# Optimization experiments

Hardware: AMD Instinct MI355X
Metric: run time of the kernel (lower is better)

## Reference

```python
import jax, jax.numpy as jnp
import numpy as np

N_WORDS, MAX_CHARS = 32768, 16
WORD_DIM, CHAR_DIM, HIDDEN = 256, 64, 256
VOCAB = 256


def setup_inputs() -> dict:
    key = jax.random.key(0)
    ks = jax.random.split(key, 10)
    char_indices = jax.random.randint(ks[0], (N_WORDS, MAX_CHARS), 0, VOCAB)
    char_lengths = jax.random.randint(ks[1], (N_WORDS,), 1, MAX_CHARS + 1)
    word_emb = jax.random.normal(ks[2], (N_WORDS, WORD_DIM), dtype=jnp.float32)
    s = 0.05
    E_char = jax.random.normal(ks[3], (VOCAB, CHAR_DIM), dtype=jnp.float32) * s
    W_ih = jax.random.normal(ks[4], (4 * HIDDEN, CHAR_DIM), dtype=jnp.float32) * s
    W_hh = jax.random.normal(ks[5], (4 * HIDDEN, HIDDEN), dtype=jnp.float32) * s
    b_ih = jax.random.normal(ks[6], (4 * HIDDEN,), dtype=jnp.float32) * s
    b_hh = jax.random.normal(ks[7], (4 * HIDDEN,), dtype=jnp.float32) * s
    W_lin = jax.random.normal(ks[8], (WORD_DIM, WORD_DIM + HIDDEN), dtype=jnp.float32) * s
    b_lin = jax.random.normal(ks[9], (WORD_DIM,), dtype=jnp.float32) * s
    return dict(char_indices=char_indices, char_lengths=char_lengths,
                word_emb=word_emb, E_char=E_char, W_ih=W_ih, W_hh=W_hh,
                b_ih=b_ih, b_hh=b_hh, W_lin=W_lin, b_lin=b_lin)


def _lstm_last_hidden(x, lengths, W_ih, W_hh, b_ih, b_hh):
    # x: [N, T, E]; returns final hidden h at position length-1 per row.
    N, T, _ = x.shape
    H = W_hh.shape[1]
    x_proj = jnp.einsum('nte,ge->ntg', x, W_ih) + (b_ih + b_hh)  # [N, T, 4H]
    x_proj = jnp.transpose(x_proj, (1, 0, 2))                    # time-major [T, N, 4H]

    def step(carry, inp):
        h, c = carry
        xg, t = inp
        gates = xg + h @ W_hh.T
        i, f, g, o = jnp.split(gates, 4, axis=-1)
        i, f, o = jax.nn.sigmoid(i), jax.nn.sigmoid(f), jax.nn.sigmoid(o)
        g = jnp.tanh(g)
        c_new = f * c + i * g
        h_new = o * jnp.tanh(c_new)
        mask = (t < lengths)[:, None]  # freeze state past each word's length
        h = jnp.where(mask, h_new, h)
        c = jnp.where(mask, c_new, c)
        return (h, c), None

    h0 = jnp.zeros((N, H), dtype=x.dtype)
    c0 = jnp.zeros((N, H), dtype=x.dtype)
    (h, _), _ = jax.lax.scan(step, (h0, c0), (x_proj, jnp.arange(T)))
    return h


def reference(char_indices, char_lengths, word_emb, E_char, W_ih, W_hh,
              b_ih, b_hh, W_lin, b_lin):
    char_embedded = E_char[char_indices]                        # [N, T, E]
    h = _lstm_last_hidden(char_embedded, char_lengths, W_ih, W_hh, b_ih, b_hh)
    combined = jnp.concatenate([word_emb, h], axis=-1)          # [N, WORD+H]
    return jax.nn.relu(combined @ W_lin.T + b_lin)              # [N, WORD]
```

## Files before the change

kernel.cpp:

```cpp
#include <hip/hip_runtime.h>


#define NW 32768

typedef __attribute__((ext_vector_type(8))) short short8;
typedef __attribute__((ext_vector_type(4))) float f32x4;
typedef __attribute__((ext_vector_type(4))) int i32x4;
typedef __attribute__((ext_vector_type(4))) unsigned short u16x4;

#define MFMA16(a,b,c) __builtin_amdgcn_mfma_f32_16x16x32_bf16(a,b,c,0,0,0)
#define MFMAI8(a,b,c) __builtin_amdgcn_mfma_i32_16x16x32_i8(a,b,c,0,0,0)

#define O_ORDER 0
#define O_SLEN  131072
#define O_WPK   262144
#define O_USTP  524288
#define O_WLIN  528384
#define O_PX    790528
#define O_BH    1314816
#define O_BASE  1323008

__device__ inline unsigned short f2b(float f) {
  unsigned u = __builtin_bit_cast(unsigned, f);
  u = u + 0x7fffu + ((u >> 16) & 1u);
  return (unsigned short)(u >> 16);
}
__device__ inline float b2f(unsigned short u) {
  return __builtin_bit_cast(float, ((unsigned)u) << 16);
}
__device__ inline float fsigm(float x) {
  float e = __builtin_amdgcn_exp2f(-1.44269504f * x);
  return __builtin_amdgcn_rcpf(1.0f + e);
}
__device__ inline float ftanh(float x) {
  float e = __builtin_amdgcn_exp2f(2.88539008f * x);
  return 1.0f - 2.0f * __builtin_amdgcn_rcpf(e + 1.0f);
}

__global__ void k_prep0(const float* __restrict__ whh, unsigned char* __restrict__ ws) {
  int i = blockIdx.x * 256 + threadIdx.x;
  const f32x4* r4 = (const f32x4*)(whh + i * 256);
  float mx = 0.f;
  #pragma unroll 8
  for (int k4 = 0; k4 < 64; ++k4) {
    f32x4 v = r4[k4];
    mx = fmaxf(mx, fmaxf(fmaxf(fabsf(v[0]), fabsf(v[1])),
                         fmaxf(fabsf(v[2]), fabsf(v[3]))));
  }
  ((float*)(ws + O_USTP))[i] = mx / (127.f * 127.f);
}

__global__ void k_prep1(const float* __restrict__ whh, const float* __restrict__ wlin,
                        unsigned char* __restrict__ ws) {
  int i = blockIdx.x * 256 + threadIdx.x;
  if (i < 262144) {
    int j = i & 7, lane = (i >> 3) & 63, t2 = i >> 9;
    int nt = t2 & 7, u2 = t2 >> 3;
    int kb = u2 & 7, w = u2 >> 3;
    int n = (nt >> 1) * 256 + w * 32 + (nt & 1) * 16 + (lane & 15);
    int k = kb * 32 + (lane >> 4) * 8 + j;
    float v = whh[n * 256 + k];
    float ustep = ((const float*)(ws + O_USTP))[n] * 127.f;
    float qf = (ustep > 0.f) ? v / ustep : 0.f;
    int q = (int)__builtin_rintf(qf);
    q = q < -127 ? -127 : (q > 127 ? 127 : q);
    ((signed char*)(ws + O_WPK))[i] = (signed char)q;
    return;
  }
  int i2 = i - 262144;
  {
    int j = i2 & 7, lane = (i2 >> 3) & 63, t3 = i2 >> 9;
    int kf = t3 & 15, nn = t3 >> 4;
    int n = (nn >> 2) * 64 + (nn & 3) * 16 + (lane & 15);
    int k = kf * 32 + (lane >> 4) * 8 + j;
    ((unsigned short*)(ws + O_WLIN))[i2] = f2b(wlin[n * 512 + k]);
  }
}

__global__ void k_prep2(const float* __restrict__ wih, const float* __restrict__ ech,
                        const float* __restrict__ bih, const float* __restrict__ bhh,
                        unsigned char* __restrict__ ws) {
  int id = blockIdx.x * 256 + threadIdx.x;
  int c = id >> 10, n = id & 1023;
  const f32x4* w4 = (const f32x4*)(wih + n * 64);
  const f32x4* e4 = (const f32x4*)(ech + c * 64);
  float acc = bih[n] + bhh[n];
  #pragma unroll
  for (int k4 = 0; k4 < 16; ++k4) {
    f32x4 a = w4[k4], e = e4[k4];
    acc += a[0] * e[0] + a[1] * e[1] + a[2] * e[2] + a[3] * e[3];
  }
  ((unsigned short*)(ws + O_PX))[((c << 8) + (n & 255)) * 4 + (n >> 8)] = f2b(acc);
}

__global__ void k_hist(const int* __restrict__ lens, unsigned char* __restrict__ ws) {
  __shared__ int h[16];
  int t = threadIdx.x, b = blockIdx.x;
  if (t < 16) h[t] = 0;
  __syncthreads();
  int wid = b * 256 + t;
  int l = lens[wid]; l = l < 1 ? 1 : (l > 16 ? 16 : l);
  atomicAdd(&h[l - 1], 1);
  __syncthreads();
  if (t < 16) ((int*)(ws + O_BH))[b * 16 + t] = h[t];
}

__global__ void k_scan(unsigned char* __restrict__ ws) {
  __shared__ int tot[16], g[16];
  int t = threadIdx.x;
  const int* bh = (const int*)(ws + O_BH);
  int* base = (int*)(ws + O_BASE);
  if (t < 16) {
    int s = 0;
    for (int b = 0; b < 128; ++b) s += bh[b * 16 + t];
    tot[t] = s;
  }
  __syncthreads();
  if (t == 0) { int a = 0; for (int i = 0; i < 16; ++i) { g[i] = a; a += tot[i]; } }
  __syncthreads();
  if (t < 16) {
    int run = g[t];
    for (int b = 0; b < 128; ++b) { base[b * 16 + t] = run; run += bh[b * 16 + t]; }
  }
}

__global__ void k_scatter(const int* __restrict__ lens, unsigned char* __restrict__ ws) {
  __shared__ int cnt[16];
  int t = threadIdx.x, b = blockIdx.x;
  if (t < 16) cnt[t] = 0;
  __syncthreads();
  int wid = b * 256 + t;
  int l = lens[wid]; l = l < 1 ? 1 : (l > 16 ? 16 : l);
  int rank = atomicAdd(&cnt[l - 1], 1);
  int p = ((const int*)(ws + O_BASE))[b * 16 + (l - 1)] + rank;
  ((int*)(ws + O_ORDER))[p] = wid;
  ((int*)(ws + O_SLEN))[p] = l;
}

__global__ __launch_bounds__(512)
__attribute__((amdgpu_waves_per_eu(2, 2)))
void k_main(
    const int* __restrict__ cidx, const float* __restrict__ wemb,
    const float* __restrict__ blin, float* __restrict__ outp,
    const unsigned char* __restrict__ ws) {
  __shared__ signed char Xb[2][4][8][64][8];
  __shared__ int CW[64][16];

  const int tid = threadIdx.x, b = blockIdx.x;
  const int w = tid >> 6, lane = tid & 63;
  const int q = lane >> 4, l15 = lane & 15;

  const int* order = (const int*)(ws + O_ORDER);
  const int* slen  = (const int*)(ws + O_SLEN);
  const signed char* wpk = (const signed char*)(ws + O_WPK);
  const float* upt = (const float*)(ws + O_USTP);
  const unsigned short* wlin = (const unsigned short*)(ws + O_WLIN);
  const unsigned short* pxt = (const unsigned short*)(ws + O_PX);

  long wreg[8][8];
  #pragma unroll
  for (int kb = 0; kb < 8; ++kb)
    #pragma unroll
    for (int nt = 0; nt < 8; ++nt)
      wreg[kb][nt] = *(const long*)(wpk + (((w * 8 + kb) * 8 + nt) * 64 + lane) * 8);

  float uq[8];
  #pragma unroll
  for (int nt = 0; nt < 8; ++nt) {
    int n = (nt >> 1) * 256 + w * 32 + (nt & 1) * 16 + l15;
    uq[nt] = upt[n];
  }
  const int hd0 = w * 32 + l15;
  const int mh = w >> 2, nw = w & 3;
  float blv[4];
  #pragma unroll
  for (int nt = 0; nt < 4; ++nt) blv[nt] = blin[nw * 64 + nt * 16 + l15];

  for (int sl = 0; sl < 2; ++sl) {
    const int s = sl ? (511 - b) : b;
    const int base = 64 * s;
    __syncthreads();
    {
      long* p = (long*)&Xb[0][0][0][0][0];
      #pragma unroll
      for (int ii = 0; ii < 4; ++ii) p[tid + 512 * ii] = 0L;
    }
    if (tid < 256) {
      int m = tid >> 2, part = tid & 3;
      int wid = order[base + m];
      *(i32x4*)&CW[m][part * 4] =
          __builtin_nontemporal_load((const i32x4*)(cidx + wid * 16 + part * 4));
    }
    int tmax[4]; unsigned lenpk[4];
    #pragma unroll
    for (int mt = 0; mt < 4; ++mt) {
      int pbm = base + 16 * mt;
      tmax[mt] = slen[pbm + 15];
      unsigned l0 = (unsigned)slen[pbm + q * 4 + 0];
      unsigned l1 = (unsigned)slen[pbm + q * 4 + 1];
      unsigned l2 = (unsigned)slen[pbm + q * 4 + 2];
      unsigned l3 = (unsigned)slen[pbm + q * 4 + 3];
      lenpk[mt] = l0 | (l1 << 8) | (l2 << 16) | (l3 << 24);
    }
    const int Tm = tmax[3];
    __syncthreads();

    float creg[4][2][4];
    unsigned hreg[4][2];
    #pragma unroll
    for (int mt = 0; mt < 4; ++mt)
      #pragma unroll
      for (int hs = 0; hs < 2; ++hs) {
        hreg[mt][hs] = 0u;
        #pragma unroll
        for (int r = 0; r < 4; ++r) creg[mt][hs][r] = 0.f;
      }

    for (int t = 0; t < Tm; ++t) {
      const int rd = t & 1, wb = rd ^ 1;
      #pragma unroll
      for (int mt = 0; mt < 4; ++mt) {
        if (mt != 3 && t >= tmax[mt]) continue;
        int cc[4];
        #pragma unroll
        for (int r = 0; r < 4; ++r) cc[r] = CW[mt * 16 + q * 4 + r][t] & 255;
        #pragma unroll
        for (int hs = 0; hs < 2; ++hs) {
          u16x4 pb[4];
          #pragma unroll
          for (int r = 0; r < 4; ++r)
            pb[r] = *(const u16x4*)&pxt[((cc[r] << 8) + hd0 + hs * 16) * 4];
          i32x4 a0 = (i32x4)0, a1 = (i32x4)0, a2 = (i32x4)0, a3 = (i32x4)0;
          #pragma unroll
          for (int kb = 0; kb < 8; ++kb) {
            long A = *(const long*)&Xb[rd][mt][kb][lane][0];
            a0 = MFMAI8(A, wreg[kb][0 + hs], a0);
            a1 = MFMAI8(A, wreg[kb][2 + hs], a1);
            a2 = MFMAI8(A, wreg[kb][4 + hs], a2);
            a3 = MFMAI8(A, wreg[kb][6 + hs], a3);
          }
          unsigned hp = 0;
          #pragma unroll
          for (int r = 0; r < 4; ++r) {
            float gi = (float)a0[r] * uq[0 + hs] + b2f(pb[r][0]);
            float gf = (float)a1[r] * uq[2 + hs] + b2f(pb[r][1]);
            float gg = (float)a2[r] * uq[4 + hs] + b2f(pb[r][2]);
            float go = (float)a3[r] * uq[6 + hs] + b2f(pb[r][3]);
            float si = fsigm(gi), sf = fsigm(gf);
            float sg = ftanh(gg), so = fsigm(go);
            float cold = creg[mt][hs][r];
            float cn = sf * cold + si * sg;
            float hn = so * ftanh(cn);
            int lene = (int)((lenpk[mt] >> (8 * r)) & 255u);
            bool live = t < lene;
            creg[mt][hs][r] = live ? cn : cold;
            int hq = (int)__builtin_rintf(127.f * hn);
            unsigned ob = (hreg[mt][hs] >> (8 * r)) & 255u;
            unsigned nb = live ? ((unsigned)hq & 255u) : ob;
            hp |= nb << (8 * r);
          }
          hreg[mt][hs] = hp;
        }
      }

      #pragma unroll
      for (int mt = 0; mt < 4; ++mt) {
        if (mt != 3 && t >= tmax[mt]) continue;
        #pragma unroll
        for (int hs = 0; hs < 2; ++hs) {
          int row16 = 16 * (hs * 2 + (l15 >> 3));
          #pragma unroll
          for (int r = 0; r < 4; ++r)
            Xb[wb][mt][w][(q * 4 + r) + row16][l15 & 7] =
                (signed char)((hreg[mt][hs] >> (8 * r)) & 255u);
        }
      }
      __syncthreads();
    }

    int widA[2];
    #pragma unroll
    for (int mi = 0; mi < 2; ++mi) widA[mi] = order[base + (2 * mh + mi) * 16 + l15];
    const int tb0 = (mh ? tmax[2] : tmax[0]) & 1;
    const int tb1 = (mh ? tmax[3] : tmax[1]) & 1;
    f32x4 fac[2][4];
    #pragma unroll
    for (int mi = 0; mi < 2; ++mi)
      #pragma unroll
      for (int nt = 0; nt < 4; ++nt) fac[mi][nt] = 0.0f;

    #pragma unroll
    for (int kf = 0; kf < 16; ++kf) {
      short8 Bn[4];
      #pragma unroll
      for (int nt = 0; nt < 4; ++nt)
        Bn[nt] = ((const short8*)wlin)[((nw * 4 + nt) * 16 + kf) * 64 + lane];
      short8 Am[2];
      #pragma unroll
      for (int mi = 0; mi < 2; ++mi) {
        if (kf < 8) {
          const f32x4* pa = (const f32x4*)(wemb + widA[mi] * 256 + kf * 32 + q * 8);
          f32x4 f0 = __builtin_nontemporal_load(pa);
          f32x4 f1 = __builtin_nontemporal_load(pa + 1);
          short8 A;
          A[0] = (short)f2b(f0[0]); A[1] = (short)f2b(f0[1]);
          A[2] = (short)f2b(f0[2]); A[3] = (short)f2b(f0[3]);
          A[4] = (short)f2b(f1[0]); A[5] = (short)f2b(f1[1]);
          A[6] = (short)f2b(f1[2]); A[7] = (short)f2b(f1[3]);
          Am[mi] = A;
        } else {
          int mtv = 2 * mh + mi;
          int tb = mi ? tb1 : tb0;
          long ch = *(const long*)&Xb[tb][mtv][kf - 8][lane][0];
          short8 A;
          #pragma unroll
          for (int j = 0; j < 8; ++j) {
            int v = (int)(signed char)((ch >> (8 * j)) & 255);
            A[j] = (short)f2b((float)v * (1.f / 127.f));
          }
          Am[mi] = A;
        }
      }
      #pragma unroll
      for (int mi = 0; mi < 2; ++mi)
        #pragma unroll
        for (int nt = 0; nt < 4; ++nt)
          fac[mi][nt] = MFMA16(Am[mi], Bn[nt], fac[mi][nt]);
    }
    #pragma unroll
    for (int mi = 0; mi < 2; ++mi) {
      #pragma unroll
      for (int r = 0; r < 4; ++r) {
        int wid = order[base + (2 * mh + mi) * 16 + q * 4 + r];
        float* po = outp + wid * 256 + nw * 64 + l15;
        #pragma unroll
        for (int nt = 0; nt < 4; ++nt) {
          float v = fac[mi][nt][r] + blv[nt];
          __builtin_nontemporal_store(v > 0.f ? v : 0.f, po + nt * 16);
        }
      }
    }
  }
}

extern "C" void kernel_launch(void* const* d_in, const int* in_sizes, int n_in,
                              void* d_out, int out_size, void* d_ws, size_t ws_size,
                              hipStream_t stream) {
  const int*   cidx = (const int*)d_in[0];
  const int*   clen = (const int*)d_in[1];
  const float* wemb = (const float*)d_in[2];
  const float* ech  = (const float*)d_in[3];
  const float* wih  = (const float*)d_in[4];
  const float* whh  = (const float*)d_in[5];
  const float* bih  = (const float*)d_in[6];
  const float* bhh  = (const float*)d_in[7];
  const float* wlin = (const float*)d_in[8];
  const float* blin = (const float*)d_in[9];
  float* outp = (float*)d_out;
  unsigned char* ws = (unsigned char*)d_ws;

  k_prep0<<<4, 256, 0, stream>>>(whh, ws);
  k_prep1<<<1536, 256, 0, stream>>>(whh, wlin, ws);
  k_prep2<<<1024, 256, 0, stream>>>(wih, ech, bih, bhh, ws);
  k_hist<<<128, 256, 0, stream>>>(clen, ws);
  k_scan<<<1, 64, 0, stream>>>(ws);
  k_scatter<<<128, 256, 0, stream>>>(clen, ws);
  k_main<<<256, 512, 0, stream>>>(cidx, wemb, blin, outp, ws);
}
```

Measured before the change: 402.5 us.

## Move half of int8 recurrent weights into LDS and single-buffer hidden state

The int8 W_hh fragments for the upper four K-blocks move from per-thread registers into a 128KB dynamic LDS region. They are reloaded from LDS every timestep, and each wave's A operands are preloaded once per tile. The double-buffered hidden-state tile becomes a single buffer, with an extra barrier between the read phase and the write phase. This halves the weight register footprint, which may ease register pressure or spilling. The cost is much more LDS read traffic per step, an additional block-wide sync per timestep, and a launch that needs about 148KB of dynamic shared memory.

```diff
diff --git a/kernel.cpp b/kernel.cpp
--- a/kernel.cpp
+++ b/kernel.cpp
@@ -143,8 +143,10 @@
     const int* __restrict__ cidx, const float* __restrict__ wemb,
     const float* __restrict__ blin, float* __restrict__ outp,
     const unsigned char* __restrict__ ws) {
-  __shared__ signed char Xb[2][4][8][64][8];
-  __shared__ int CW[64][16];
+  extern __shared__ signed char smem[];
+  signed char (*WL)[8][8][64][8] = (signed char (*)[8][8][64][8])smem;
+  signed char (*Xb)[8][64][8] = (signed char (*)[8][64][8])(smem + 131072);
+  int (*CW)[16] = (int (*)[16])(smem + 131072 + 16384);
 
   const int tid = threadIdx.x, b = blockIdx.x;
   const int w = tid >> 6, lane = tid & 63;
@@ -157,12 +159,25 @@
   const unsigned short* wlin = (const unsigned short*)(ws + O_WLIN);
   const unsigned short* pxt = (const unsigned short*)(ws + O_PX);
 
-  long wreg[8][8];
+  long wreg[4][8];
   #pragma unroll
-  for (int kb = 0; kb < 8; ++kb)
+  for (int kb = 0; kb < 4; ++kb)
     #pragma unroll
     for (int nt = 0; nt < 8; ++nt)
       wreg[kb][nt] = *(const long*)(wpk + (((w * 8 + kb) * 8 + nt) * 64 + lane) * 8);
+
+  {
+    long* wlds = (long*)smem;
+    const long* wsrc = (const long*)wpk;
+    #pragma unroll
+    for (int ii = 0; ii < 32; ++ii) {
+      int f = ii * 512 + tid;
+      int lane_ = f & 63, r = f >> 6;
+      int nt_ = r & 7, r2 = r >> 3;
+      int w_ = r2 & 7, kb4 = r2 >> 3;
+      wlds[f] = wsrc[((w_ * 8 + 4 + kb4) * 8 + nt_) * 64 + lane_];
+    }
+  }
 
   float uq[8];
   #pragma unroll
@@ -181,7 +196,7 @@
     const int base = 64 * s;
     __syncthreads();
     {
-      long* p = (long*)&Xb[0][0][0][0][0];
+      long* p = (long*)&Xb[0][0][0][0];
       #pragma unroll
       for (int ii = 0; ii < 4; ++ii) p[tid + 512 * ii] = 0L;
     }
@@ -217,10 +232,13 @@
       }
 
     for (int t = 0; t < Tm; ++t) {
-      const int rd = t & 1, wb = rd ^ 1;
       #pragma unroll
       for (int mt = 0; mt < 4; ++mt) {
         if (mt != 3 && t >= tmax[mt]) continue;
+        long Ar[8];
+        #pragma unroll
+        for (int kb = 0; kb < 8; ++kb)
+          Ar[kb] = *(const long*)&Xb[mt][kb][lane][0];
         int cc[4];
         #pragma unroll
         for (int r = 0; r < 4; ++r) cc[r] = CW[mt * 16 + q * 4 + r][t] & 255;
@@ -232,12 +250,22 @@
             pb[r] = *(const u16x4*)&pxt[((cc[r] << 8) + hd0 + hs * 16) * 4];
           i32x4 a0 = (i32x4)0, a1 = (i32x4)0, a2 = (i32x4)0, a3 = (i32x4)0;
           #pragma unroll
-          for (int kb = 0; kb < 8; ++kb) {
-            long A = *(const long*)&Xb[rd][mt][kb][lane][0];
-            a0 = MFMAI8(A, wreg[kb][0 + hs], a0);
-            a1 = MFMAI8(A, wreg[kb][2 + hs], a1);
-            a2 = MFMAI8(A, wreg[kb][4 + hs], a2);
-            a3 = MFMAI8(A, wreg[kb][6 + hs], a3);
+          for (int kb = 0; kb < 4; ++kb) {
+            a0 = MFMAI8(Ar[kb], wreg[kb][0 + hs], a0);
+            a1 = MFMAI8(Ar[kb], wreg[kb][2 + hs], a1);
+            a2 = MFMAI8(Ar[kb], wreg[kb][4 + hs], a2);
+            a3 = MFMAI8(Ar[kb], wreg[kb][6 + hs], a3);
+          }
+          #pragma unroll
+          for (int kb = 4; kb < 8; ++kb) {
+            long b0 = *(const long*)&WL[kb - 4][w][0 + hs][lane][0];
+            long b1 = *(const long*)&WL[kb - 4][w][2 + hs][lane][0];
+            long b2 = *(const long*)&WL[kb - 4][w][4 + hs][lane][0];
+            long b3 = *(const long*)&WL[kb - 4][w][6 + hs][lane][0];
+            a0 = MFMAI8(Ar[kb], b0, a0);
+            a1 = MFMAI8(Ar[kb], b1, a1);
+            a2 = MFMAI8(Ar[kb], b2, a2);
+            a3 = MFMAI8(Ar[kb], b3, a3);
           }
           unsigned hp = 0;
           #pragma unroll
@@ -262,6 +290,7 @@
           hreg[mt][hs] = hp;
         }
       }
+      __syncthreads();
 
       #pragma unroll
       for (int mt = 0; mt < 4; ++mt) {
@@ -271,7 +300,7 @@
           int row16 = 16 * (hs * 2 + (l15 >> 3));
           #pragma unroll
           for (int r = 0; r < 4; ++r)
-            Xb[wb][mt][w][(q * 4 + r) + row16][l15 & 7] =
+            Xb[mt][w][(q * 4 + r) + row16][l15 & 7] =
                 (signed char)((hreg[mt][hs] >> (8 * r)) & 255u);
         }
       }
@@ -281,8 +310,6 @@
     int widA[2];
     #pragma unroll
     for (int mi = 0; mi < 2; ++mi) widA[mi] = order[base + (2 * mh + mi) * 16 + l15];
-    const int tb0 = (mh ? tmax[2] : tmax[0]) & 1;
-    const int tb1 = (mh ? tmax[3] : tmax[1]) & 1;
     f32x4 fac[2][4];
     #pragma unroll
     for (int mi = 0; mi < 2; ++mi)
@@ -310,8 +337,7 @@
           Am[mi] = A;
         } else {
           int mtv = 2 * mh + mi;
-          int tb = mi ? tb1 : tb0;
-          long ch = *(const long*)&Xb[tb][mtv][kf - 8][lane][0];
+          long ch = *(const long*)&Xb[mtv][kf - 8][lane][0];
           short8 A;
           #pragma unroll
           for (int j = 0; j < 8; ++j) {
@@ -365,5 +391,5 @@
   k_hist<<<128, 256, 0, stream>>>(clen, ws);
   k_scan<<<1, 64, 0, stream>>>(ws);
   k_scatter<<<128, 256, 0, stream>>>(clen, ws);
-  k_main<<<256, 512, 0, stream>>>(cidx, wemb, blin, outp, ws);
-}
+  k_main<<<256, 512, 151552, stream>>>(cidx, wemb, blin, outp, ws);
+}
```

Measured after the change: 399.1 us. No clear change (-0.8%).

## Merge prep kernels and use atomic work-queue scheduling in main kernel

Applied to the files above, without the earlier changes.

Five small prep kernels become two launches, cutting launch overhead. The main kernel now pulls 64-word slices from a global atomic counter, starting with the longest-length slices, instead of taking a fixed pair per block. It launches 512 blocks and declares waves_per_eu 4, which may squeeze registers for the 64-long weight array and cause spills. The word-embedding loads also drop the nontemporal hint.

```diff
diff --git a/kernel.cpp b/kernel.cpp
--- a/kernel.cpp
+++ b/kernel.cpp
@@ -19,6 +19,7 @@
 #define O_PX    790528
 #define O_BH    1314816
 #define O_BASE  1323008
+#define O_CTR   1331200
 
 __device__ inline unsigned short f2b(float f) {
   unsigned u = __builtin_bit_cast(unsigned, f);
@@ -37,22 +38,72 @@
   return 1.0f - 2.0f * __builtin_amdgcn_rcpf(e + 1.0f);
 }
 
-__global__ void k_prep0(const float* __restrict__ whh, unsigned char* __restrict__ ws) {
-  int i = blockIdx.x * 256 + threadIdx.x;
-  const f32x4* r4 = (const f32x4*)(whh + i * 256);
-  float mx = 0.f;
-  #pragma unroll 8
-  for (int k4 = 0; k4 < 64; ++k4) {
-    f32x4 v = r4[k4];
-    mx = fmaxf(mx, fmaxf(fmaxf(fabsf(v[0]), fabsf(v[1])),
-                         fmaxf(fabsf(v[2]), fabsf(v[3]))));
-  }
-  ((float*)(ws + O_USTP))[i] = mx / (127.f * 127.f);
-}
-
-__global__ void k_prep1(const float* __restrict__ whh, const float* __restrict__ wlin,
+__global__ void k_prepA(const float* __restrict__ whh, const int* __restrict__ lens,
+                        const float* __restrict__ wih, const float* __restrict__ ech,
+                        const float* __restrict__ bih, const float* __restrict__ bhh,
                         unsigned char* __restrict__ ws) {
-  int i = blockIdx.x * 256 + threadIdx.x;
+  int bid = blockIdx.x, tid = threadIdx.x;
+  if (bid == 0 && tid == 0) *(int*)(ws + O_CTR) = 0;
+  if (bid < 4) {
+    int i = bid * 256 + tid;
+    const f32x4* r4 = (const f32x4*)(whh + i * 256);
+    float mx = 0.f;
+    #pragma unroll 8
+    for (int k4 = 0; k4 < 64; ++k4) {
+      f32x4 v = r4[k4];
+      mx = fmaxf(mx, fmaxf(fmaxf(fabsf(v[0]), fabsf(v[1])),
+                           fmaxf(fabsf(v[2]), fabsf(v[3]))));
+    }
+    ((float*)(ws + O_USTP))[i] = mx / (127.f * 127.f);
+    return;
+  }
+  if (bid < 132) {
+    __shared__ int h[16];
+    int b2 = bid - 4;
+    if (tid < 16) h[tid] = 0;
+    __syncthreads();
+    int wid = b2 * 256 + tid;
+    int l = lens[wid]; l = l < 1 ? 1 : (l > 16 ? 16 : l);
+    atomicAdd(&h[l - 1], 1);
+    __syncthreads();
+    if (tid < 16) ((int*)(ws + O_BH))[b2 * 16 + tid] = h[tid];
+    return;
+  }
+  int id = (bid - 132) * 256 + tid;
+  int c = id >> 10, n = id & 1023;
+  const f32x4* w4 = (const f32x4*)(wih + n * 64);
+  const f32x4* e4 = (const f32x4*)(ech + c * 64);
+  float acc = bih[n] + bhh[n];
+  #pragma unroll
+  for (int k4 = 0; k4 < 16; ++k4) {
+    f32x4 a = w4[k4], e = e4[k4];
+    acc += a[0] * e[0] + a[1] * e[1] + a[2] * e[2] + a[3] * e[3];
+  }
+  ((unsigned short*)(ws + O_PX))[((c << 8) + (n & 255)) * 4 + (n >> 8)] = f2b(acc);
+}
+
+__global__ void k_prepB(const float* __restrict__ whh, const float* __restrict__ wlin,
+                        unsigned char* __restrict__ ws) {
+  int bid = blockIdx.x, tid = threadIdx.x;
+  if (bid == 0) {
+    __shared__ int tot[16], g[16];
+    const int* bh = (const int*)(ws + O_BH);
+    int* base = (int*)(ws + O_BASE);
+    if (tid < 16) {
+      int s = 0;
+      for (int b = 0; b < 128; ++b) s += bh[b * 16 + tid];
+      tot[tid] = s;
+    }
+    __syncthreads();
+    if (tid == 0) { int a = 0; for (int i = 0; i < 16; ++i) { g[i] = a; a += tot[i]; } }
+    __syncthreads();
+    if (tid < 16) {
+      int run = g[tid];
+      for (int b = 0; b < 128; ++b) { base[b * 16 + tid] = run; run += bh[b * 16 + tid]; }
+    }
+    return;
+  }
+  int i = (bid - 1) * 256 + tid;
   if (i < 262144) {
     int j = i & 7, lane = (i >> 3) & 63, t2 = i >> 9;
     int nt = t2 & 7, u2 = t2 >> 3;
@@ -77,53 +128,6 @@
   }
 }
 
-__global__ void k_prep2(const float* __restrict__ wih, const float* __restrict__ ech,
-                        const float* __restrict__ bih, const float* __restrict__ bhh,
-                        unsigned char* __restrict__ ws) {
-  int id = blockIdx.x * 256 + threadIdx.x;
-  int c = id >> 10, n = id & 1023;
-  const f32x4* w4 = (const f32x4*)(wih + n * 64);
-  const f32x4* e4 = (const f32x4*)(ech + c * 64);
-  float acc = bih[n] + bhh[n];
-  #pragma unroll
-  for (int k4 = 0; k4 < 16; ++k4) {
-    f32x4 a = w4[k4], e = e4[k4];
-    acc += a[0] * e[0] + a[1] * e[1] + a[2] * e[2] + a[3] * e[3];
-  }
-  ((unsigned short*)(ws + O_PX))[((c << 8) + (n & 255)) * 4 + (n >> 8)] = f2b(acc);
-}
-
-__global__ void k_hist(const int* __restrict__ lens, unsigned char* __restrict__ ws) {
-  __shared__ int h[16];
-  int t = threadIdx.x, b = blockIdx.x;
-  if (t < 16) h[t] = 0;
-  __syncthreads();
-  int wid = b * 256 + t;
-  int l = lens[wid]; l = l < 1 ? 1 : (l > 16 ? 16 : l);
-  atomicAdd(&h[l - 1], 1);
-  __syncthreads();
-  if (t < 16) ((int*)(ws + O_BH))[b * 16 + t] = h[t];
-}
-
-__global__ void k_scan(unsigned char* __restrict__ ws) {
-  __shared__ int tot[16], g[16];
-  int t = threadIdx.x;
-  const int* bh = (const int*)(ws + O_BH);
-  int* base = (int*)(ws + O_BASE);
-  if (t < 16) {
-    int s = 0;
-    for (int b = 0; b < 128; ++b) s += bh[b * 16 + t];
-    tot[t] = s;
-  }
-  __syncthreads();
-  if (t == 0) { int a = 0; for (int i = 0; i < 16; ++i) { g[i] = a; a += tot[i]; } }
-  __syncthreads();
-  if (t < 16) {
-    int run = g[t];
-    for (int b = 0; b < 128; ++b) { base[b * 16 + t] = run; run += bh[b * 16 + t]; }
-  }
-}
-
 __global__ void k_scatter(const int* __restrict__ lens, unsigned char* __restrict__ ws) {
   __shared__ int cnt[16];
   int t = threadIdx.x, b = blockIdx.x;
@@ -138,15 +142,16 @@
 }
 
 __global__ __launch_bounds__(512)
-__attribute__((amdgpu_waves_per_eu(2, 2)))
+__attribute__((amdgpu_waves_per_eu(4, 4)))
 void k_main(
     const int* __restrict__ cidx, const float* __restrict__ wemb,
     const float* __restrict__ blin, float* __restrict__ outp,
-    const unsigned char* __restrict__ ws) {
+    unsigned char* __restrict__ ws) {
   __shared__ signed char Xb[2][4][8][64][8];
   __shared__ int CW[64][16];
-
-  const int tid = threadIdx.x, b = blockIdx.x;
+  __shared__ int s_slice;
+
+  const int tid = threadIdx.x;
   const int w = tid >> 6, lane = tid & 63;
   const int q = lane >> 4, l15 = lane & 15;
 
@@ -176,14 +181,18 @@
   #pragma unroll
   for (int nt = 0; nt < 4; ++nt) blv[nt] = blin[nw * 64 + nt * 16 + l15];
 
-  for (int sl = 0; sl < 2; ++sl) {
-    const int s = sl ? (511 - b) : b;
+  for (;;) {
+    if (tid == 0) s_slice = atomicAdd((int*)(ws + O_CTR), 1);
+    __syncthreads();
+    const int p = s_slice;
+    if (p >= 512) break;
+    const int s = 511 - p;
     const int base = 64 * s;
-    __syncthreads();
+
     {
-      long* p = (long*)&Xb[0][0][0][0][0];
-      #pragma unroll
-      for (int ii = 0; ii < 4; ++ii) p[tid + 512 * ii] = 0L;
+      long* pz = (long*)&Xb[0][0][0][0][0];
+      #pragma unroll
+      for (int ii = 0; ii < 4; ++ii) pz[tid + 512 * ii] = 0L;
     }
     if (tid < 256) {
       int m = tid >> 2, part = tid & 3;
@@ -300,8 +309,8 @@
       for (int mi = 0; mi < 2; ++mi) {
         if (kf < 8) {
           const f32x4* pa = (const f32x4*)(wemb + widA[mi] * 256 + kf * 32 + q * 8);
-          f32x4 f0 = __builtin_nontemporal_load(pa);
-          f32x4 f1 = __builtin_nontemporal_load(pa + 1);
+          f32x4 f0 = pa[0];
+          f32x4 f1 = pa[1];
           short8 A;
           A[0] = (short)f2b(f0[0]); A[1] = (short)f2b(f0[1]);
           A[2] = (short)f2b(f0[2]); A[3] = (short)f2b(f0[3]);
@@ -359,11 +368,8 @@
   float* outp = (float*)d_out;
   unsigned char* ws = (unsigned char*)d_ws;
 
-  k_prep0<<<4, 256, 0, stream>>>(whh, ws);
-  k_prep1<<<1536, 256, 0, stream>>>(whh, wlin, ws);
-  k_prep2<<<1024, 256, 0, stream>>>(wih, ech, bih, bhh, ws);
-  k_hist<<<128, 256, 0, stream>>>(clen, ws);
-  k_scan<<<1, 64, 0, stream>>>(ws);
+  k_prepA<<<1156, 256, 0, stream>>>(whh, clen, wih, ech, bih, bhh, ws);
+  k_prepB<<<1537, 256, 0, stream>>>(whh, wlin, ws);
   k_scatter<<<128, 256, 0, stream>>>(clen, ws);
-  k_main<<<256, 512, 0, stream>>>(cidx, wemb, blin, outp, ws);
-}
+  k_main<<<512, 512, 0, stream>>>(cidx, wemb, blin, outp, ws);
+}
```

Measured after the change: 1.205 ms. 2.99x slower.
